# Kernel optimization log

Measured on AMD Instinct MI355X. Metric: run time of the kernel, lower is better.

The kernel has to match this reference:

```python
import jax, jax.numpy as jnp
import numpy as np

TAU = 0.1
HARD_K = 32
MIN_OVERLAP = 4
PAIR_WEIGHTS = [("view", "cart", 0.2), ("cart", "purchase", 1.0), ("view", "purchase", 1.0)]


def setup_inputs() -> dict:
    key = jax.random.key(0)
    ks = jax.random.split(key, 6)
    U, D = 100000, 128
    return {
        "emb_view": jax.random.normal(ks[0], (U, D), dtype=jnp.float32),
        "emb_cart": jax.random.normal(ks[1], (U, D), dtype=jnp.float32),
        "emb_purchase": jax.random.normal(ks[2], (U, D), dtype=jnp.float32),
        "users_view": jax.random.randint(ks[3], (20000,), 0, U, dtype=jnp.int64),
        "users_cart": jax.random.randint(ks[4], (15000,), 0, U, dtype=jnp.int64),
        "users_purchase": jax.random.randint(ks[5], (10000,), 0, U, dtype=jnp.int64),
    }


def _l2norm(x):
    # F.normalize(x, dim=-1): x / max(||x||, eps)
    n = jnp.linalg.norm(x, axis=-1, keepdims=True)
    return x / jnp.maximum(n, 1e-12)


def _directional(z_weak, z_strong, tau, hard_k):
    N = z_strong.shape[0]
    if N < 2:
        return jnp.zeros((), dtype=z_strong.dtype)
    z_w = _l2norm(jax.lax.stop_gradient(z_weak))  # weak side is detached
    z_s = _l2norm(z_strong)
    sim = (z_s @ z_w.T) / tau  # [N, N]
    pos = jnp.diagonal(sim)    # positive logits, labels = arange(N)
    n_hard = min(hard_k, N - 1)
    if 0 < n_hard < N - 1:
        neg_only = jnp.where(jnp.eye(N, dtype=bool), -jnp.inf, sim)
        hard_neg, _ = jax.lax.top_k(neg_only, n_hard)          # [N, n_hard]
        logits = jnp.concatenate([pos[:, None], hard_neg], 1)  # [N, 1+n_hard]
        return jnp.mean(jax.scipy.special.logsumexp(logits, axis=1) - pos)
    # full-softmax CE with label i for row i
    return jnp.mean(jax.scipy.special.logsumexp(sim, axis=1) - pos)


def reference(emb_view, emb_cart, emb_purchase, users_view, users_cart, users_purchase):
    embs = {"view": emb_view, "cart": emb_cart, "purchase": emb_purchase}
    users = {
        "view": np.asarray(users_view),
        "cart": np.asarray(users_cart),
        "purchase": np.asarray(users_purchase),
    }
    loss = jnp.zeros((), dtype=emb_view.dtype)
    for weak, strong, w in PAIR_WEIGHTS:
        u_w, u_s = users[weak], users[strong]
        if u_w.size == 0 or u_s.size == 0:
            continue
        # common_pair = u_w[isin(u_w, u_s)] : keeps u_w order and duplicates
        common = u_w[np.isin(u_w, u_s)]
        if common.size < MIN_OVERLAP:
            continue
        idx = jnp.asarray(common)
        loss = loss + w * _directional(embs[weak][idx], embs[strong][idx], TAU, HARD_K)
    return loss
```

## Files before the change

### kernel.cpp

```cpp
#include <hip/hip_runtime.h>
#include <hip/hip_bf16.h>
#include <math.h>

#define D 128
#define NEG_INF (-3.0e38f)
#define LDA 136
#define MAGIC 0x5CA1AB1Eu

#define C0 3200
#define C1 1792
#define C2 2304
#define T0 25
#define T1 14
#define T2 18
#define NTILES (T0 * T0 + T1 * T1 + T2 * T2)
#define NSEL (C0 / 4 + C1 / 4 + C2 / 4)

typedef __attribute__((ext_vector_type(8))) short bf16x8;
typedef __attribute__((ext_vector_type(8))) unsigned short u16x8;
typedef __attribute__((ext_vector_type(4))) float f32x4;

__device__ __forceinline__ float wredf_add(float v) {
#pragma unroll
  for (int m = 32; m; m >>= 1) v += __shfl_xor(v, m, 64);
  return v;
}
__device__ __forceinline__ float wredf_max(float v) {
#pragma unroll
  for (int m = 32; m; m >>= 1) v = fmaxf(v, __shfl_xor(v, m, 64));
  return v;
}
__device__ __forceinline__ float wredf_min(float v) {
#pragma unroll
  for (int m = 32; m; m >>= 1) v = fminf(v, __shfl_xor(v, m, 64));
  return v;
}
__device__ __forceinline__ int wredi_add(int v) {
#pragma unroll
  for (int m = 32; m; m >>= 1) v += __shfl_xor(v, m, 64);
  return v;
}
__device__ __forceinline__ double wredd_add(double v) {
#pragma unroll
  for (int m = 32; m; m >>= 1) v += __shfl_xor(v, m, 64);
  return v;
}

__global__ void masks_k(const int* __restrict__ uc, int nc,
                        const int* __restrict__ up, int npu,
                        unsigned* __restrict__ mc, unsigned* __restrict__ mp,
                        unsigned long long* __restrict__ header) {
  if (blockIdx.x == 0) header[threadIdx.x] = 0ull;
  int t = blockIdx.x * blockDim.x + threadIdx.x;
  if (t < nc) {
    mc[uc[t]] = MAGIC;
  } else {
    int t2 = t - nc;
    if (t2 < npu) mp[up[t2]] = MAGIC;
  }
}

struct FGArgs {
  const int* src[3];
  int n[3];
  const unsigned* mask[3];
  const float* embW[3];
  const float* embS[3];
  short* zw[3];
  short* zs[3];
  int cap[3];
  int seg1, seg2;
  int* counts;
};

__global__ __launch_bounds__(256) void filtgather_k(FGArgs a) {
  int t = blockIdx.x * 256 + threadIdx.x;
  int lane = threadIdx.x & 63;
  int s, base;
  if (t < a.seg1) { s = 0; base = t; }
  else if (t < a.seg2) { s = 1; base = t - a.seg1; }
  else { s = 2; base = t - a.seg2; }
  bool match = false;
  int u = 0;
  if (base < a.n[s]) {
    u = a.src[s][base];
    match = (a.mask[s][u] == MAGIC);
  }
  unsigned long long b = __ballot(match);
  int tot = __popcll(b);
  if (!tot) return;
  int idx0 = 0;
  if (lane == 0) idx0 = atomicAdd(a.counts + s, tot);
  idx0 = __shfl(idx0, 0, 64);
  const float* eW = a.embW[s];
  const float* eS = a.embS[s];
  short* zw = a.zw[s];
  short* zs = a.zs[s];
  int cap = a.cap[s];
  unsigned long long bb = b;
  for (int k = 0; k < tot; ++k) {
    int sl = __builtin_ctzll(bb);
    bb &= bb - 1;
    int p = idx0 + k;
    if (p >= cap) break;
    int uu = __shfl(u, sl, 64);
    float2 vw = *(const float2*)(eW + (size_t)uu * D + lane * 2);
    float2 vs = *(const float2*)(eS + (size_t)uu * D + lane * 2);
    float ssw = wredf_add(vw.x * vw.x + vw.y * vw.y);
    float sss = wredf_add(vs.x * vs.x + vs.y * vs.y);
    float iw = 1.0f / fmaxf(sqrtf(ssw), 1e-12f);
    float is = 1.0f / fmaxf(sqrtf(sss), 1e-12f);
    __hip_bfloat16 w0 = __float2bfloat16(vw.x * iw), w1 = __float2bfloat16(vw.y * iw);
    __hip_bfloat16 s0 = __float2bfloat16(vs.x * is), s1 = __float2bfloat16(vs.y * is);
    *(ushort2*)(zw + (size_t)p * D + lane * 2) =
        make_ushort2(*(unsigned short*)&w0, *(unsigned short*)&w1);
    *(ushort2*)(zs + (size_t)p * D + lane * 2) =
        make_ushort2(*(unsigned short*)&s0, *(unsigned short*)&s1);
  }
}

struct GemmArgs {
  const short *zs0, *zw0, *zs1, *zw1, *zs2, *zw2;
  unsigned short *s0, *s1, *s2;
  const int* counts;
};

__device__ __forceinline__ void gemm_tile(const short* __restrict__ A, const short* __restrict__ B,
                                          unsigned short* __restrict__ C, int ldc, int bx, int by,
                                          int N, short* As, short* Bs, int tid) {
  int rb = by * 128, cb = bx * 128;
  if (rb >= N || cb >= N) return;
  int rrow = tid >> 4, rcol = (tid & 15) * 8;
#pragma unroll
  for (int pass = 0; pass < 8; ++pass) {
    int row = pass * 16 + rrow;
    uint4 va = *(const uint4*)(A + (size_t)(rb + row) * D + rcol);
    uint4 vb = *(const uint4*)(B + (size_t)(cb + row) * D + rcol);
    *(uint4*)(&As[row * LDA + rcol]) = va;
    *(uint4*)(&Bs[row * LDA + rcol]) = vb;
  }
  __syncthreads();
  int wave = tid >> 6, lane = tid & 63;
  int wr = (wave >> 1) * 64, wc = (wave & 1) * 64;
  int ln = lane & 15, quad = lane >> 4;
  f32x4 acc[4][4] = {};
#pragma unroll
  for (int ks = 0; ks < 4; ++ks) {
    int ko = ks * 32 + quad * 8;
    bf16x8 af[4], bg[4];
#pragma unroll
    for (int i = 0; i < 4; ++i) af[i] = *(const bf16x8*)(&As[(wr + i * 16 + ln) * LDA + ko]);
#pragma unroll
    for (int j = 0; j < 4; ++j) bg[j] = *(const bf16x8*)(&Bs[(wc + j * 16 + ln) * LDA + ko]);
#pragma unroll
    for (int i = 0; i < 4; ++i)
#pragma unroll
      for (int j = 0; j < 4; ++j)
        acc[i][j] = __builtin_amdgcn_mfma_f32_16x16x32_bf16(af[i], bg[j], acc[i][j], 0, 0, 0);
  }
  __syncthreads();
#pragma unroll
  for (int i = 0; i < 4; ++i)
#pragma unroll
    for (int j = 0; j < 4; ++j) {
      int tcol = wc + j * 16 + ln;
#pragma unroll
      for (int r = 0; r < 4; ++r) {
        int trow = wr + i * 16 + quad * 4 + r;
        __hip_bfloat16 h = __float2bfloat16(acc[i][j][r] * 10.0f);
        As[trow * LDA + tcol] = *(short*)&h;
      }
    }
  __syncthreads();
#pragma unroll
  for (int pass = 0; pass < 8; ++pass) {
    int idx = pass * 256 + tid;
    int row = idx >> 4, c8 = (idx & 15) * 8;
    *(uint4*)(C + (size_t)(rb + row) * ldc + cb + c8) = *(const uint4*)(&As[row * LDA + c8]);
  }
  __syncthreads();
}

__global__ __launch_bounds__(256) void gemm_all_k(GemmArgs g) {
  __shared__ __align__(16) short As[128 * LDA];
  __shared__ __align__(16) short Bs[128 * LDA];
  int tid = threadIdx.x;
  int b = blockIdx.x;
  if (b < T0 * T0) {
    int N = min(g.counts[0], C0);
    gemm_tile(g.zs0, g.zw0, g.s0, C0, b % T0, b / T0, N, As, Bs, tid);
  } else if (b < T0 * T0 + T1 * T1) {
    int t = b - T0 * T0;
    int N = min(g.counts[1], C1);
    gemm_tile(g.zs1, g.zw1, g.s1, C1, t % T1, t / T1, N, As, Bs, tid);
  } else {
    int t = b - T0 * T0 - T1 * T1;
    int N = min(g.counts[2], C2);
    gemm_tile(g.zs2, g.zw2, g.s2, C2, t % T2, t / T2, N, As, Bs, tid);
  }
}

template <int NL>
__device__ __forceinline__ void select_rows(const unsigned short* __restrict__ sim, int ldc, int N,
                                            int i, int lane, double* __restrict__ slot) {
  const unsigned short* row = sim + (size_t)i * ldc;
  float vals[NL * 8];
  float posl = NEG_INF;
#pragma unroll
  for (int L = 0; L < NL; ++L) {
    int base = L * 512 + lane * 8;
    u16x8 raw = *(const u16x8*)(row + base);
#pragma unroll
    for (int c = 0; c < 8; ++c) {
      int j = base + c;
      float v = __uint_as_float((unsigned)raw[c] << 16);
      if (L >= NL - 2 && j >= N) v = NEG_INF;
      if (j == i) { posl = v; v = NEG_INF; }
      vals[L * 8 + c] = v;
    }
  }
  float pos = __shfl(posl, (i >> 3) & 63, 64);
  float m = NEG_INF;
#pragma unroll
  for (int s = 0; s < NL * 8; ++s) m = fmaxf(m, vals[s]);
  m = wredf_max(m);
  int K = min(32, N - 1);
  float lo = -10.2f, hi = m + 1e-3f;
  for (int it = 0; it < 12; ++it) {
    float mid = 0.5f * (lo + hi);
    int c = 0;
#pragma unroll
    for (int s = 0; s < NL * 8; ++s) c += (vals[s] > mid) ? 1 : 0;
    c = wredi_add(c);
    if (c >= K) lo = mid; else hi = mid;
  }
  float M = fmaxf(m, pos);
  float sum = 0.0f, vmin = 3.0e38f;
  int cnt = 0;
#pragma unroll
  for (int s = 0; s < NL * 8; ++s) {
    float v = vals[s];
    if (v > lo) {
      sum += __expf(v - M);
      cnt++;
      vmin = fminf(vmin, v);
    }
  }
  sum = wredf_add(sum);
  cnt = wredi_add(cnt);
  vmin = wredf_min(vmin);
  float corr = (cnt > K) ? (float)(cnt - K) * __expf(vmin - M) : 0.0f;
  float lse = M + __logf(sum - corr + __expf(pos - M));
  if (lane == 0) atomicAdd(slot, (double)(lse - pos));
}

__global__ __launch_bounds__(256) void select_k(const unsigned short* __restrict__ sim0,
                                                const unsigned short* __restrict__ sim1,
                                                const unsigned short* __restrict__ sim2,
                                                const int* __restrict__ counts,
                                                double* __restrict__ partials) {
  int wid = threadIdx.x >> 6, lane = threadIdx.x & 63;
  int b = blockIdx.x;
  if (b < C0 / 4) {
    int N = min(counts[0], C0);
    int i = b * 4 + wid;
    if (i < N) {
      double* slot = partials + 0 * 64 + (b & 63);
      if (N <= 3072) select_rows<6>(sim0, C0, N, i, lane, slot);
      else           select_rows<7>(sim0, C0, N, i, lane, slot);
    }
  } else if (b < C0 / 4 + C1 / 4) {
    int bb = b - C0 / 4;
    int N = min(counts[1], C1);
    int i = bb * 4 + wid;
    if (i < N) {
      double* slot = partials + 64 + (bb & 63);
      if (N <= 1536) select_rows<3>(sim1, C1, N, i, lane, slot);
      else           select_rows<4>(sim1, C1, N, i, lane, slot);
    }
  } else {
    int bb = b - C0 / 4 - C1 / 4;
    int N = min(counts[2], C2);
    int i = bb * 4 + wid;
    if (i < N) {
      double* slot = partials + 128 + (bb & 63);
      if (N <= 2048) select_rows<4>(sim2, C2, N, i, lane, slot);
      else           select_rows<5>(sim2, C2, N, i, lane, slot);
    }
  }
}

__global__ void finalize_k(const int* __restrict__ counts, const double* __restrict__ partials,
                           float* __restrict__ out) {
  int wid = threadIdx.x >> 6, lane = threadIdx.x & 63;
  __shared__ double ps[4];
  double v = (threadIdx.x < 192) ? partials[threadIdx.x] : 0.0;
  v = wredd_add(v);
  if (lane == 0 && wid < 3) ps[wid] = v;
  __syncthreads();
  if (threadIdx.x == 0) {
    const float w[3] = {0.2f, 1.0f, 1.0f};
    const int caps[3] = {C0, C1, C2};
    float tot = 0.0f;
    for (int p = 0; p < 3; ++p) {
      int N = min(counts[p], caps[p]);
      if (N >= 4) tot += w[p] * (float)(ps[p] / (double)N);
    }
    out[0] = tot;
  }
}

__global__ void sentinel_k(float* out) {
  if (threadIdx.x == 0 && blockIdx.x == 0) out[0] = -12345.0f;
}

extern "C" void kernel_launch(void* const* d_in, const int* in_sizes, int n_in,
                              void* d_out, int out_size, void* d_ws, size_t ws_size,
                              hipStream_t stream) {
  const float* emb_view = (const float*)d_in[0];
  const float* emb_cart = (const float*)d_in[1];
  const float* emb_pur  = (const float*)d_in[2];
  const int* u_view = (const int*)d_in[3];
  const int* u_cart = (const int*)d_in[4];
  const int* u_pur  = (const int*)d_in[5];
  int nv = in_sizes[3], nc = in_sizes[4], np = in_sizes[5];
  int U = in_sizes[0] / D;

  size_t off = 2048;
  auto alloc = [&](size_t b) {
    size_t o = (off + 255) & ~(size_t)255;
    off = o + b;
    return o;
  };
  size_t mask0_off = alloc((size_t)U * 4);
  size_t mask1_off = alloc((size_t)U * 4);
  size_t zw0_off = alloc((size_t)C0 * D * 2);
  size_t zs0_off = alloc((size_t)C0 * D * 2);
  size_t zw1_off = alloc((size_t)C1 * D * 2);
  size_t zs1_off = alloc((size_t)C1 * D * 2);
  size_t zw2_off = alloc((size_t)C2 * D * 2);
  size_t zs2_off = alloc((size_t)C2 * D * 2);
  size_t sim0_off = alloc((size_t)C0 * C0 * 2);
  size_t sim1_off = alloc((size_t)C1 * C1 * 2);
  size_t sim2_off = alloc((size_t)C2 * C2 * 2);
  (void)alloc(1024);
  int ws_ok = (off <= ws_size) ? 1 : 0;

  char* ws = (char*)d_ws;
  if (!ws_ok) {
    sentinel_k<<<1, 1, 0, stream>>>((float*)d_out);
    return;
  }

  int* counts = (int*)ws;
  double* partials = (double*)(ws + 256);
  unsigned* mask_c = (unsigned*)(ws + mask0_off);
  unsigned* mask_p = (unsigned*)(ws + mask1_off);
  short* zw0 = (short*)(ws + zw0_off);
  short* zs0 = (short*)(ws + zs0_off);
  short* zw1 = (short*)(ws + zw1_off);
  short* zs1 = (short*)(ws + zs1_off);
  short* zw2 = (short*)(ws + zw2_off);
  short* zs2 = (short*)(ws + zs2_off);
  unsigned short* sim0 = (unsigned short*)(ws + sim0_off);
  unsigned short* sim1 = (unsigned short*)(ws + sim1_off);
  unsigned short* sim2 = (unsigned short*)(ws + sim2_off);

  masks_k<<<(nc + np + 255) / 256, 256, 0, stream>>>(u_cart, nc, u_pur, np, mask_c, mask_p,
                                                     (unsigned long long*)ws);

  FGArgs fa;
  fa.src[0] = u_view; fa.n[0] = nv; fa.mask[0] = mask_c;
  fa.embW[0] = emb_view; fa.embS[0] = emb_cart; fa.zw[0] = zw0; fa.zs[0] = zs0; fa.cap[0] = C0;
  fa.src[1] = u_cart; fa.n[1] = nc; fa.mask[1] = mask_p;
  fa.embW[1] = emb_cart; fa.embS[1] = emb_pur; fa.zw[1] = zw1; fa.zs[1] = zs1; fa.cap[1] = C1;
  fa.src[2] = u_view; fa.n[2] = nv; fa.mask[2] = mask_p;
  fa.embW[2] = emb_view; fa.embS[2] = emb_pur; fa.zw[2] = zw2; fa.zs[2] = zs2; fa.cap[2] = C2;
  fa.seg1 = ((nv + 255) / 256) * 256;
  fa.seg2 = fa.seg1 + ((nc + 255) / 256) * 256;
  int t_filt = fa.seg2 + ((nv + 255) / 256) * 256;
  fa.counts = counts;
  filtgather_k<<<t_filt / 256, 256, 0, stream>>>(fa);

  GemmArgs g;
  g.zs0 = zs0; g.zw0 = zw0; g.s0 = sim0;
  g.zs1 = zs1; g.zw1 = zw1; g.s1 = sim1;
  g.zs2 = zs2; g.zw2 = zw2; g.s2 = sim2;
  g.counts = counts;
  gemm_all_k<<<NTILES, 256, 0, stream>>>(g);

  select_k<<<NSEL, 256, 0, stream>>>(sim0, sim1, sim2, counts, partials);

  finalize_k<<<1, 256, 0, stream>>>(counts, partials, (float*)d_out);
}
```

Before: 212.0 us.

## Load GEMM B operand from global, ballot-based counting, fuse finalize into select

```diff
diff --git a/kernel.cpp b/kernel.cpp
--- a/kernel.cpp
+++ b/kernel.cpp
@@ -33,11 +33,6 @@
 __device__ __forceinline__ float wredf_min(float v) {
 #pragma unroll
   for (int m = 32; m; m >>= 1) v = fminf(v, __shfl_xor(v, m, 64));
-  return v;
-}
-__device__ __forceinline__ int wredi_add(int v) {
-#pragma unroll
-  for (int m = 32; m; m >>= 1) v += __shfl_xor(v, m, 64);
   return v;
 }
 __device__ __forceinline__ double wredd_add(double v) {
@@ -127,17 +122,14 @@
 
 __device__ __forceinline__ void gemm_tile(const short* __restrict__ A, const short* __restrict__ B,
                                           unsigned short* __restrict__ C, int ldc, int bx, int by,
-                                          int N, short* As, short* Bs, int tid) {
+                                          int N, short* As, int tid) {
   int rb = by * 128, cb = bx * 128;
   if (rb >= N || cb >= N) return;
   int rrow = tid >> 4, rcol = (tid & 15) * 8;
 #pragma unroll
   for (int pass = 0; pass < 8; ++pass) {
     int row = pass * 16 + rrow;
-    uint4 va = *(const uint4*)(A + (size_t)(rb + row) * D + rcol);
-    uint4 vb = *(const uint4*)(B + (size_t)(cb + row) * D + rcol);
-    *(uint4*)(&As[row * LDA + rcol]) = va;
-    *(uint4*)(&Bs[row * LDA + rcol]) = vb;
+    *(uint4*)(&As[row * LDA + rcol]) = *(const uint4*)(A + (size_t)(rb + row) * D + rcol);
   }
   __syncthreads();
   int wave = tid >> 6, lane = tid & 63;
@@ -149,9 +141,10 @@
     int ko = ks * 32 + quad * 8;
     bf16x8 af[4], bg[4];
 #pragma unroll
+    for (int j = 0; j < 4; ++j)
+      bg[j] = *(const bf16x8*)(B + (size_t)(cb + wc + j * 16 + ln) * D + ko);
+#pragma unroll
     for (int i = 0; i < 4; ++i) af[i] = *(const bf16x8*)(&As[(wr + i * 16 + ln) * LDA + ko]);
-#pragma unroll
-    for (int j = 0; j < 4; ++j) bg[j] = *(const bf16x8*)(&Bs[(wc + j * 16 + ln) * LDA + ko]);
 #pragma unroll
     for (int i = 0; i < 4; ++i)
 #pragma unroll
@@ -178,25 +171,23 @@
     int row = idx >> 4, c8 = (idx & 15) * 8;
     *(uint4*)(C + (size_t)(rb + row) * ldc + cb + c8) = *(const uint4*)(&As[row * LDA + c8]);
   }
-  __syncthreads();
-}
-
-__global__ __launch_bounds__(256) void gemm_all_k(GemmArgs g) {
+}
+
+__global__ __launch_bounds__(256, 4) void gemm_all_k(GemmArgs g) {
   __shared__ __align__(16) short As[128 * LDA];
-  __shared__ __align__(16) short Bs[128 * LDA];
   int tid = threadIdx.x;
   int b = blockIdx.x;
   if (b < T0 * T0) {
     int N = min(g.counts[0], C0);
-    gemm_tile(g.zs0, g.zw0, g.s0, C0, b % T0, b / T0, N, As, Bs, tid);
+    gemm_tile(g.zs0, g.zw0, g.s0, C0, b % T0, b / T0, N, As, tid);
   } else if (b < T0 * T0 + T1 * T1) {
     int t = b - T0 * T0;
     int N = min(g.counts[1], C1);
-    gemm_tile(g.zs1, g.zw1, g.s1, C1, t % T1, t / T1, N, As, Bs, tid);
+    gemm_tile(g.zs1, g.zw1, g.s1, C1, t % T1, t / T1, N, As, tid);
   } else {
     int t = b - T0 * T0 - T1 * T1;
     int N = min(g.counts[2], C2);
-    gemm_tile(g.zs2, g.zw2, g.s2, C2, t % T2, t / T2, N, As, Bs, tid);
+    gemm_tile(g.zs2, g.zw2, g.s2, C2, t % T2, t / T2, N, As, tid);
   }
 }
 
@@ -230,8 +221,7 @@
     float mid = 0.5f * (lo + hi);
     int c = 0;
 #pragma unroll
-    for (int s = 0; s < NL * 8; ++s) c += (vals[s] > mid) ? 1 : 0;
-    c = wredi_add(c);
+    for (int s = 0; s < NL * 8; ++s) c += (int)__popcll(__ballot(vals[s] > mid));
     if (c >= K) lo = mid; else hi = mid;
   }
   float M = fmaxf(m, pos);
@@ -240,14 +230,14 @@
 #pragma unroll
   for (int s = 0; s < NL * 8; ++s) {
     float v = vals[s];
-    if (v > lo) {
+    bool sel = (v > lo);
+    cnt += (int)__popcll(__ballot(sel));
+    if (sel) {
       sum += __expf(v - M);
-      cnt++;
       vmin = fminf(vmin, v);
     }
   }
   sum = wredf_add(sum);
-  cnt = wredi_add(cnt);
   vmin = wredf_min(vmin);
   float corr = (cnt > K) ? (float)(cnt - K) * __expf(vmin - M) : 0.0f;
   float lse = M + __logf(sum - corr + __expf(pos - M));
@@ -258,7 +248,9 @@
                                                 const unsigned short* __restrict__ sim1,
                                                 const unsigned short* __restrict__ sim2,
                                                 const int* __restrict__ counts,
-                                                double* __restrict__ partials) {
+                                                double* __restrict__ partials,
+                                                int* __restrict__ sel_done,
+                                                float* __restrict__ out) {
   int wid = threadIdx.x >> 6, lane = threadIdx.x & 63;
   int b = blockIdx.x;
   if (b < C0 / 4) {
@@ -288,25 +280,31 @@
       else           select_rows<5>(sim2, C2, N, i, lane, slot);
     }
   }
-}
-
-__global__ void finalize_k(const int* __restrict__ counts, const double* __restrict__ partials,
-                           float* __restrict__ out) {
-  int wid = threadIdx.x >> 6, lane = threadIdx.x & 63;
+  __threadfence();
+  __shared__ int s_last;
   __shared__ double ps[4];
-  double v = (threadIdx.x < 192) ? partials[threadIdx.x] : 0.0;
-  v = wredd_add(v);
-  if (lane == 0 && wid < 3) ps[wid] = v;
+  if (threadIdx.x == 0)
+    s_last = (atomicAdd(sel_done, 1) == NSEL - 1) ? 1 : 0;
   __syncthreads();
-  if (threadIdx.x == 0) {
-    const float w[3] = {0.2f, 1.0f, 1.0f};
-    const int caps[3] = {C0, C1, C2};
-    float tot = 0.0f;
-    for (int p = 0; p < 3; ++p) {
-      int N = min(counts[p], caps[p]);
-      if (N >= 4) tot += w[p] * (float)(ps[p] / (double)N);
-    }
-    out[0] = tot;
+  if (s_last) {
+    __threadfence();
+    int tid = threadIdx.x;
+    double v = (tid < 192)
+                   ? __hip_atomic_load(&partials[tid], __ATOMIC_RELAXED, __HIP_MEMORY_SCOPE_AGENT)
+                   : 0.0;
+    v = wredd_add(v);
+    if (lane == 0 && wid < 3) ps[wid] = v;
+    __syncthreads();
+    if (tid == 0) {
+      const float w[3] = {0.2f, 1.0f, 1.0f};
+      const int caps[3] = {C0, C1, C2};
+      float tot = 0.0f;
+      for (int p = 0; p < 3; ++p) {
+        int N = min(counts[p], caps[p]);
+        if (N >= 4) tot += w[p] * (float)(ps[p] / (double)N);
+      }
+      out[0] = tot;
+    }
   }
 }
 
@@ -353,6 +351,7 @@
   }
 
   int* counts = (int*)ws;
+  int* sel_done = (int*)(ws + 128);
   double* partials = (double*)(ws + 256);
   unsigned* mask_c = (unsigned*)(ws + mask0_off);
   unsigned* mask_p = (unsigned*)(ws + mask1_off);
@@ -389,7 +388,6 @@
   g.counts = counts;
   gemm_all_k<<<NTILES, 256, 0, stream>>>(g);
 
-  select_k<<<NSEL, 256, 0, stream>>>(sim0, sim1, sim2, counts, partials);
-
-  finalize_k<<<1, 256, 0, stream>>>(counts, partials, (float*)d_out);
-}
+  select_k<<<NSEL, 256, 0, stream>>>(sim0, sim1, sim2, counts, partials, sel_done,
+                                     (float*)d_out);
+}
```

Measured after the change: 317.2 us. +49.6%, slower.
